# Kernel tuning notes

Hardware: AMD Instinct MI355X
Metric: run time of the kernel (lower is better)

## Reference

```python
import jax, jax.numpy as jnp
import numpy as np

B, H, W, D = 4, 64, 64, 256
NH = 8
HD = D // NH        # 32
R = 2               # reduction_ratio
SCALE = 1.0 / np.sqrt(HD).astype(np.float32)
EPS = 1e-5


def _layernorm(x, g, b):
    m = jnp.mean(x, axis=-1, keepdims=True)
    v = jnp.mean((x - m) ** 2, axis=-1, keepdims=True)
    return (x - m) * jax.lax.rsqrt(v + EPS) * g + b


def setup_inputs() -> dict:
    key = jax.random.key(0)
    ks = jax.random.split(key, 8)
    s = 0.02
    return {
        "x": jax.random.normal(ks[0], (B, H, W, D), jnp.float32),
        "de": jax.random.normal(ks[1], (B, H, W, D), jnp.float32),  # unused by module
        "ln1_g": jnp.ones((D,), jnp.float32),
        "ln1_b": jnp.zeros((D,), jnp.float32),
        "Wq": jax.random.normal(ks[2], (D, D), jnp.float32) * s,
        "bq": jnp.zeros((D,), jnp.float32),
        "Wk": jax.random.normal(ks[3], (D, D), jnp.float32) * s,
        "bk": jnp.zeros((D,), jnp.float32),
        "Wv": jax.random.normal(ks[4], (D, D), jnp.float32) * s,
        "bv": jnp.zeros((D,), jnp.float32),
        "Wmean": jax.random.normal(ks[5], (D, D), jnp.float32) * s,  # no bias
        "ln2_g": jnp.ones((D,), jnp.float32),
        "ln2_b": jnp.zeros((D,), jnp.float32),
        "Wo": jax.random.normal(ks[6], (D, D), jnp.float32) * s,
        "bo": jnp.zeros((D,), jnp.float32),
    }


def reference(x, de, ln1_g, ln1_b, Wq, bq, Wk, bk, Wv, bv, Wmean, ln2_g, ln2_b, Wo, bo):
    b, h, w, d = x.shape
    identity = x
    x_norm = _layernorm(x, ln1_g, ln1_b)
    q = x_norm @ Wq + bq                                   # [b,h,w,d]
    # shift_size == 0 -> no roll. Block-mean pool K/V by factor R.
    x_red = jnp.mean(x.reshape(b, h // R, R, w // R, R, d), axis=(2, 4))  # [b,h/R,w/R,d]
    x_red = x_red @ Wmean
    x_red_norm = _layernorm(x_red, ln2_g, ln2_b)
    k = x_red_norm @ Wk + bk
    v = x_red_norm @ Wv + bv
    # split heads: [b, NH, N, HD]
    qf = q.reshape(b, h * w, NH, HD).transpose(0, 2, 1, 3)
    kf = k.reshape(b, (h // R) * (w // R), NH, HD).transpose(0, 2, 1, 3)
    vf = v.reshape(b, (h // R) * (w // R), NH, HD).transpose(0, 2, 1, 3)
    attn = jax.nn.softmax(jnp.einsum('bhqd,bhkd->bhqk', qf, kf) * SCALE, axis=-1)
    out = jnp.einsum('bhqk,bhkd->bhqd', attn, vf)          # [b,NH,N,HD]
    out = out.transpose(0, 2, 1, 3).reshape(b, h, w, d)
    out = out @ Wo + bo
    out = out + identity
    return out, attn
```

## Files before the change

### kernel.cpp

```cpp
#include <hip/hip_runtime.h>

typedef __bf16 bf16x8 __attribute__((ext_vector_type(8)));
typedef __bf16 bf16x4 __attribute__((ext_vector_type(4)));
typedef float f32x4 __attribute__((ext_vector_type(4)));

#define SCALE 0.17677669529663687f

__global__ __launch_bounds__(256) void castw_kernel(
    const float* __restrict__ W0, const float* __restrict__ W1,
    const float* __restrict__ W2, const float* __restrict__ W3,
    const float* __restrict__ W4,
    __bf16* __restrict__ T0, __bf16* __restrict__ T1,
    __bf16* __restrict__ T2, __bf16* __restrict__ T3,
    __bf16* __restrict__ T4) {
  int which = blockIdx.x >> 8;
  const float* W = which == 0 ? W0 : which == 1 ? W1 : which == 2 ? W2 : which == 3 ? W3 : W4;
  __bf16* T = which == 0 ? T0 : which == 1 ? T1 : which == 2 ? T2 : which == 3 ? T3 : T4;
  int id = (blockIdx.x & 255) * 256 + threadIdx.x;
  int kk = id >> 8, n = id & 255;
  T[n * 256 + kk] = (__bf16)W[id];
}

__global__ __launch_bounds__(256) void ln_fp32_kernel(const float* __restrict__ in,
    const float* __restrict__ g, const float* __restrict__ bb,
    __bf16* __restrict__ out) {
  int wid = (blockIdx.x * 256 + threadIdx.x) >> 6;
  int lane = threadIdx.x & 63;
  const float4 v = *(const float4*)(in + (size_t)wid * 256 + lane * 4);
  float s = v.x + v.y + v.z + v.w;
  #pragma unroll
  for (int off = 32; off; off >>= 1) s += __shfl_down(s, off);
  float mean = __shfl(s, 0) * (1.0f / 256.0f);
  float dx = v.x - mean, dy = v.y - mean, dz = v.z - mean, dw = v.w - mean;
  float vs = dx * dx + dy * dy + dz * dz + dw * dw;
  #pragma unroll
  for (int off = 32; off; off >>= 1) vs += __shfl_down(vs, off);
  float rstd = rsqrtf(__shfl(vs, 0) * (1.0f / 256.0f) + 1e-5f);
  const float4 gg = *(const float4*)(g + lane * 4);
  const float4 bv = *(const float4*)(bb + lane * 4);
  bf16x4 o4;
  o4[0] = (__bf16)(dx * rstd * gg.x + bv.x);
  o4[1] = (__bf16)(dy * rstd * gg.y + bv.y);
  o4[2] = (__bf16)(dz * rstd * gg.z + bv.z);
  o4[3] = (__bf16)(dw * rstd * gg.w + bv.w);
  *(bf16x4*)(out + (size_t)wid * 256 + lane * 4) = o4;
}

__global__ __launch_bounds__(256) void ln_bf16_kernel(const __bf16* __restrict__ in,
    const float* __restrict__ g, const float* __restrict__ bb,
    __bf16* __restrict__ out) {
  int wid = (blockIdx.x * 256 + threadIdx.x) >> 6;
  int lane = threadIdx.x & 63;
  bf16x4 iv = *(const bf16x4*)(in + (size_t)wid * 256 + lane * 4);
  float vx = (float)iv[0], vy = (float)iv[1], vz = (float)iv[2], vw = (float)iv[3];
  float s = vx + vy + vz + vw;
  #pragma unroll
  for (int off = 32; off; off >>= 1) s += __shfl_down(s, off);
  float mean = __shfl(s, 0) * (1.0f / 256.0f);
  float dx = vx - mean, dy = vy - mean, dz = vz - mean, dw = vw - mean;
  float vs = dx * dx + dy * dy + dz * dz + dw * dw;
  #pragma unroll
  for (int off = 32; off; off >>= 1) vs += __shfl_down(vs, off);
  float rstd = rsqrtf(__shfl(vs, 0) * (1.0f / 256.0f) + 1e-5f);
  const float4 gg = *(const float4*)(g + lane * 4);
  const float4 bv = *(const float4*)(bb + lane * 4);
  bf16x4 o4;
  o4[0] = (__bf16)(dx * rstd * gg.x + bv.x);
  o4[1] = (__bf16)(dy * rstd * gg.y + bv.y);
  o4[2] = (__bf16)(dz * rstd * gg.z + bv.z);
  o4[3] = (__bf16)(dw * rstd * gg.w + bv.w);
  *(bf16x4*)(out + (size_t)wid * 256 + lane * 4) = o4;
}

__global__ __launch_bounds__(256) void pool_kernel(const float* __restrict__ x,
    __bf16* __restrict__ xp) {
  int idx = blockIdx.x * 256 + threadIdx.x;
  int t = idx >> 6, c4 = (idx & 63) << 2;
  int b = t >> 10, rem = t & 1023;
  int i = rem >> 5, j = rem & 31;
  size_t base = ((size_t)b * 4096 + i * 128 + j * 2) * 256 + c4;
  float4 a0 = *(const float4*)(x + base);
  float4 a1 = *(const float4*)(x + base + 256);
  float4 a2 = *(const float4*)(x + base + 16384);
  float4 a3 = *(const float4*)(x + base + 16640);
  bf16x4 o4;
  o4[0] = (__bf16)(0.25f * (a0.x + a1.x + a2.x + a3.x));
  o4[1] = (__bf16)(0.25f * (a0.y + a1.y + a2.y + a3.y));
  o4[2] = (__bf16)(0.25f * (a0.z + a1.z + a2.z + a3.z));
  o4[3] = (__bf16)(0.25f * (a0.w + a1.w + a2.w + a3.w));
  *(bf16x4*)(xp + (size_t)t * 256 + c4) = o4;
}

__global__ __launch_bounds__(256) void gemm_mfma(
    const __bf16* __restrict__ A, const __bf16* __restrict__ Wt,
    const float* __restrict__ bias, const float* __restrict__ resid,
    void* __restrict__ Cout, int mode) {
  const int tid = threadIdx.x;
  const int w = tid >> 6, l = tid & 63;
  const int col = l & 15, quad = l >> 4;
  const int row0 = blockIdx.x * 64 + w * 16;
  const int col0 = blockIdx.y * 64;
  f32x4 acc[4] = {{0.f,0.f,0.f,0.f},{0.f,0.f,0.f,0.f},{0.f,0.f,0.f,0.f},{0.f,0.f,0.f,0.f}};
  const __bf16* ap = A + (size_t)(row0 + col) * 256 + quad * 8;
  #pragma unroll
  for (int ks = 0; ks < 8; ++ks) {
    bf16x8 af = *(const bf16x8*)(ap + ks * 32);
    #pragma unroll
    for (int n = 0; n < 4; ++n) {
      bf16x8 bf = *(const bf16x8*)(Wt + (size_t)(col0 + n * 16 + col) * 256 + ks * 32 + quad * 8);
      acc[n] = __builtin_amdgcn_mfma_f32_16x16x32_bf16(af, bf, acc[n], 0, 0, 0);
    }
  }
  const int rbase = row0 + quad * 4;
  #pragma unroll
  for (int n = 0; n < 4; ++n) {
    const int cc = col0 + n * 16 + col;
    const float bv = bias ? bias[cc] : 0.0f;
    if (mode == 0) {
      __bf16* C = (__bf16*)Cout;
      #pragma unroll
      for (int r = 0; r < 4; ++r)
        C[(size_t)(rbase + r) * 256 + cc] = (__bf16)(acc[n][r] + bv);
    } else if (mode == 1) {
      __bf16* C = (__bf16*)Cout;
      const int bb2 = rbase >> 10, tl = rbase & 1023;
      bf16x4 o4;
      #pragma unroll
      for (int r = 0; r < 4; ++r) o4[r] = (__bf16)(acc[n][r] + bv);
      *(bf16x4*)(C + ((size_t)(bb2 * 256 + cc)) * 1024 + tl) = o4;
    } else {
      float* C = (float*)Cout;
      #pragma unroll
      for (int r = 0; r < 4; ++r) {
        size_t off = (size_t)(rbase + r) * 256 + cc;
        C[off] = acc[n][r] + bv + resid[off];
      }
    }
  }
}

__device__ __forceinline__ int swz(int row, int c) {
  return row * 1024 + (c ^ ((row & 7) << 2));
}

__global__ __launch_bounds__(256) void attn_fused(
    const __bf16* __restrict__ q, const __bf16* __restrict__ kb,
    const __bf16* __restrict__ vT, float* __restrict__ attn,
    __bf16* __restrict__ oat) {
  __shared__ float Ss[16 * 1024];
  __shared__ float part[64 * 32];
  __shared__ float inv_s[16];
  const int tid = threadIdx.x;
  const int w = tid >> 6, l = tid & 63;
  const int col = l & 15, quad = l >> 4;
  const int bh = blockIdx.y, b = bh >> 3, h = bh & 7;
  const int q0 = blockIdx.x * 16;

  bf16x8 qf = *(const bf16x8*)(q + ((size_t)(b * 4096 + q0 + col)) * 256 + h * 32 + quad * 8);
  const __bf16* kbase = kb + ((size_t)(b * 1024 + col)) * 256 + h * 32 + quad * 8;
  #pragma unroll 4
  for (int t = 0; t < 16; ++t) {
    int j0 = w * 256 + t * 16;
    bf16x8 kf = *(const bf16x8*)(kbase + (size_t)j0 * 256);
    f32x4 c = {0.f, 0.f, 0.f, 0.f};
    c = __builtin_amdgcn_mfma_f32_16x16x32_bf16(qf, kf, c, 0, 0, 0);
    #pragma unroll
    for (int r = 0; r < 4; ++r)
      Ss[swz(quad * 4 + r, j0 + col)] = c[r] * SCALE;
  }
  __syncthreads();

  #pragma unroll
  for (int rr = 0; rr < 4; ++rr) {
    int row = w * 4 + rr;
    float4 v4[4];
    float m = -1e30f;
    #pragma unroll
    for (int i = 0; i < 4; ++i) {
      v4[i] = *(const float4*)(&Ss[swz(row, i * 256 + l * 4)]);
      m = fmaxf(m, fmaxf(fmaxf(v4[i].x, v4[i].y), fmaxf(v4[i].z, v4[i].w)));
    }
    #pragma unroll
    for (int off = 32; off; off >>= 1) m = fmaxf(m, __shfl_down(m, off));
    m = __shfl(m, 0);
    float s = 0.f;
    #pragma unroll
    for (int i = 0; i < 4; ++i) {
      v4[i].x = __expf(v4[i].x - m); v4[i].y = __expf(v4[i].y - m);
      v4[i].z = __expf(v4[i].z - m); v4[i].w = __expf(v4[i].w - m);
      s += v4[i].x + v4[i].y + v4[i].z + v4[i].w;
    }
    #pragma unroll
    for (int off = 32; off; off >>= 1) s += __shfl_down(s, off);
    if (l == 0) inv_s[row] = 1.0f / __shfl(s, 0);
    #pragma unroll
    for (int i = 0; i < 4; ++i)
      *(float4*)(&Ss[swz(row, i * 256 + l * 4)]) = v4[i];
  }
  __syncthreads();

  f32x4 a0 = {0.f, 0.f, 0.f, 0.f}, a1 = {0.f, 0.f, 0.f, 0.f};
  const __bf16* v0p = vT + ((size_t)(b * 256 + h * 32 + col)) * 1024;
  const __bf16* v1p = v0p + 16 * 1024;
  #pragma unroll 2
  for (int s8 = 0; s8 < 8; ++s8) {
    int k0 = w * 256 + s8 * 32;
    int c0 = k0 + quad * 8;
    f32x4 p0 = *(const f32x4*)(&Ss[swz(col, c0)]);
    f32x4 p1 = *(const f32x4*)(&Ss[swz(col, c0 + 4)]);
    bf16x8 af;
    af[0] = (__bf16)p0[0]; af[1] = (__bf16)p0[1]; af[2] = (__bf16)p0[2]; af[3] = (__bf16)p0[3];
    af[4] = (__bf16)p1[0]; af[5] = (__bf16)p1[1]; af[6] = (__bf16)p1[2]; af[7] = (__bf16)p1[3];
    bf16x8 b0 = *(const bf16x8*)(v0p + k0 + quad * 8);
    bf16x8 b1 = *(const bf16x8*)(v1p + k0 + quad * 8);
    a0 = __builtin_amdgcn_mfma_f32_16x16x32_bf16(af, b0, a0, 0, 0, 0);
    a1 = __builtin_amdgcn_mfma_f32_16x16x32_bf16(af, b1, a1, 0, 0, 0);
  }

  #pragma unroll
  for (int r = 0; r < 4; ++r) {
    part[(w * 16 + quad * 4 + r) * 32 + col] = a0[r];
    part[(w * 16 + quad * 4 + r) * 32 + 16 + col] = a1[r];
  }
  __syncthreads();
  int idx = tid;
  #pragma unroll
  for (int it = 0; it < 2; ++it, idx += 256) {
    int row = idx >> 5, d = idx & 31;
    float sum = (part[row * 32 + d] + part[(16 + row) * 32 + d]
               + part[(32 + row) * 32 + d] + part[(48 + row) * 32 + d]) * inv_s[row];
    oat[((size_t)(b * 4096 + q0 + row)) * 256 + h * 32 + d] = (__bf16)sum;
  }

  float* abase = attn + ((size_t)bh * 4096 + q0) * 1024;
  int c4 = tid * 4;
  #pragma unroll 4
  for (int row = 0; row < 16; ++row) {
    f32x4 pv = *(const f32x4*)(&Ss[swz(row, c4)]);
    float iv = inv_s[row];
    pv[0] *= iv; pv[1] *= iv; pv[2] *= iv; pv[3] *= iv;
    __builtin_nontemporal_store(pv, (f32x4*)(abase + (size_t)row * 1024 + c4));
  }
}

extern "C" void kernel_launch(void* const* d_in, const int* in_sizes, int n_in,
                              void* d_out, int out_size, void* d_ws, size_t ws_size,
                              hipStream_t stream) {
  (void)in_sizes; (void)n_in; (void)out_size; (void)ws_size;
  const float* x     = (const float*)d_in[0];
  const float* ln1_g = (const float*)d_in[2];
  const float* ln1_b = (const float*)d_in[3];
  const float* Wq    = (const float*)d_in[4];
  const float* bq    = (const float*)d_in[5];
  const float* Wk    = (const float*)d_in[6];
  const float* bk    = (const float*)d_in[7];
  const float* Wv    = (const float*)d_in[8];
  const float* bv    = (const float*)d_in[9];
  const float* Wmean = (const float*)d_in[10];
  const float* ln2_g = (const float*)d_in[11];
  const float* ln2_b = (const float*)d_in[12];
  const float* Wo    = (const float*)d_in[13];
  const float* bo    = (const float*)d_in[14];

  float* out  = (float*)d_out;
  float* attn = out + 4194304;

  __bf16* w0   = (__bf16*)d_ws;
  __bf16* xn   = w0;
  __bf16* qb   = w0 + 4194304;
  __bf16* oat  = w0 + 8388608;
  __bf16* xp   = w0 + 12582912;
  __bf16* xrm  = w0 + 13631488;
  __bf16* xr   = w0 + 14680064;
  __bf16* kbuf = w0 + 15728640;
  __bf16* vTb  = w0 + 16777216;
  __bf16* WtQ  = w0 + 17825792;
  __bf16* WtK  = WtQ + 65536;
  __bf16* WtV  = WtK + 65536;
  __bf16* WtM  = WtV + 65536;
  __bf16* WtO  = WtM + 65536;

  castw_kernel<<<1280, 256, 0, stream>>>(Wq, Wk, Wv, Wmean, Wo, WtQ, WtK, WtV, WtM, WtO);

  ln_fp32_kernel<<<4096, 256, 0, stream>>>(x, ln1_g, ln1_b, xn);
  gemm_mfma<<<dim3(256, 4), 256, 0, stream>>>(xn, WtQ, bq, nullptr, qb, 0);
  pool_kernel<<<1024, 256, 0, stream>>>(x, xp);
  gemm_mfma<<<dim3(64, 4), 256, 0, stream>>>(xp, WtM, nullptr, nullptr, xrm, 0);
  ln_bf16_kernel<<<1024, 256, 0, stream>>>(xrm, ln2_g, ln2_b, xr);
  gemm_mfma<<<dim3(64, 4), 256, 0, stream>>>(xr, WtK, bk, nullptr, kbuf, 0);
  gemm_mfma<<<dim3(64, 4), 256, 0, stream>>>(xr, WtV, bv, nullptr, vTb, 1);
  attn_fused<<<dim3(256, 32), 256, 0, stream>>>(qb, kbuf, vTb, attn, oat);
  gemm_mfma<<<dim3(256, 4), 256, 0, stream>>>(oat, WtO, bo, x, (void*)out, 2);
}
```

Before: 741.0 us.

## Merge prep kernels, fuse Wmean GEMM with LayerNorm, and batch K/V GEMMs

Reduces ten launches to five. The weight cast, LN1 and pooling now run as one block-partitioned kernel. The Q projection shares a launch with a Wmean GEMM that computes full 256-wide rows per warp and applies LN2 in registers, which removes the xrm round trip and the separate LN kernel. K and V GEMMs share one launch. The attention kernel now writes the attn matrix before the PV MFMA loop, which may overlap the big store with compute, and the GEMM mode becomes a template parameter. The fused Wmean path uses 16 accumulators per lane, which raises register pressure, and its per-element bf16 stores are uncoalesced.

Result: no change. 744.9 us (+0.5%).

```diff
diff --git a/kernel.cpp b/kernel.cpp
--- a/kernel.cpp
+++ b/kernel.cpp
@@ -6,100 +6,15 @@
 
 #define SCALE 0.17677669529663687f
 
-__global__ __launch_bounds__(256) void castw_kernel(
-    const float* __restrict__ W0, const float* __restrict__ W1,
-    const float* __restrict__ W2, const float* __restrict__ W3,
-    const float* __restrict__ W4,
-    __bf16* __restrict__ T0, __bf16* __restrict__ T1,
-    __bf16* __restrict__ T2, __bf16* __restrict__ T3,
-    __bf16* __restrict__ T4) {
-  int which = blockIdx.x >> 8;
-  const float* W = which == 0 ? W0 : which == 1 ? W1 : which == 2 ? W2 : which == 3 ? W3 : W4;
-  __bf16* T = which == 0 ? T0 : which == 1 ? T1 : which == 2 ? T2 : which == 3 ? T3 : T4;
-  int id = (blockIdx.x & 255) * 256 + threadIdx.x;
-  int kk = id >> 8, n = id & 255;
-  T[n * 256 + kk] = (__bf16)W[id];
-}
-
-__global__ __launch_bounds__(256) void ln_fp32_kernel(const float* __restrict__ in,
-    const float* __restrict__ g, const float* __restrict__ bb,
-    __bf16* __restrict__ out) {
-  int wid = (blockIdx.x * 256 + threadIdx.x) >> 6;
-  int lane = threadIdx.x & 63;
-  const float4 v = *(const float4*)(in + (size_t)wid * 256 + lane * 4);
-  float s = v.x + v.y + v.z + v.w;
-  #pragma unroll
-  for (int off = 32; off; off >>= 1) s += __shfl_down(s, off);
-  float mean = __shfl(s, 0) * (1.0f / 256.0f);
-  float dx = v.x - mean, dy = v.y - mean, dz = v.z - mean, dw = v.w - mean;
-  float vs = dx * dx + dy * dy + dz * dz + dw * dw;
-  #pragma unroll
-  for (int off = 32; off; off >>= 1) vs += __shfl_down(vs, off);
-  float rstd = rsqrtf(__shfl(vs, 0) * (1.0f / 256.0f) + 1e-5f);
-  const float4 gg = *(const float4*)(g + lane * 4);
-  const float4 bv = *(const float4*)(bb + lane * 4);
-  bf16x4 o4;
-  o4[0] = (__bf16)(dx * rstd * gg.x + bv.x);
-  o4[1] = (__bf16)(dy * rstd * gg.y + bv.y);
-  o4[2] = (__bf16)(dz * rstd * gg.z + bv.z);
-  o4[3] = (__bf16)(dw * rstd * gg.w + bv.w);
-  *(bf16x4*)(out + (size_t)wid * 256 + lane * 4) = o4;
-}
-
-__global__ __launch_bounds__(256) void ln_bf16_kernel(const __bf16* __restrict__ in,
-    const float* __restrict__ g, const float* __restrict__ bb,
-    __bf16* __restrict__ out) {
-  int wid = (blockIdx.x * 256 + threadIdx.x) >> 6;
-  int lane = threadIdx.x & 63;
-  bf16x4 iv = *(const bf16x4*)(in + (size_t)wid * 256 + lane * 4);
-  float vx = (float)iv[0], vy = (float)iv[1], vz = (float)iv[2], vw = (float)iv[3];
-  float s = vx + vy + vz + vw;
-  #pragma unroll
-  for (int off = 32; off; off >>= 1) s += __shfl_down(s, off);
-  float mean = __shfl(s, 0) * (1.0f / 256.0f);
-  float dx = vx - mean, dy = vy - mean, dz = vz - mean, dw = vw - mean;
-  float vs = dx * dx + dy * dy + dz * dz + dw * dw;
-  #pragma unroll
-  for (int off = 32; off; off >>= 1) vs += __shfl_down(vs, off);
-  float rstd = rsqrtf(__shfl(vs, 0) * (1.0f / 256.0f) + 1e-5f);
-  const float4 gg = *(const float4*)(g + lane * 4);
-  const float4 bv = *(const float4*)(bb + lane * 4);
-  bf16x4 o4;
-  o4[0] = (__bf16)(dx * rstd * gg.x + bv.x);
-  o4[1] = (__bf16)(dy * rstd * gg.y + bv.y);
-  o4[2] = (__bf16)(dz * rstd * gg.z + bv.z);
-  o4[3] = (__bf16)(dw * rstd * gg.w + bv.w);
-  *(bf16x4*)(out + (size_t)wid * 256 + lane * 4) = o4;
-}
-
-__global__ __launch_bounds__(256) void pool_kernel(const float* __restrict__ x,
-    __bf16* __restrict__ xp) {
-  int idx = blockIdx.x * 256 + threadIdx.x;
-  int t = idx >> 6, c4 = (idx & 63) << 2;
-  int b = t >> 10, rem = t & 1023;
-  int i = rem >> 5, j = rem & 31;
-  size_t base = ((size_t)b * 4096 + i * 128 + j * 2) * 256 + c4;
-  float4 a0 = *(const float4*)(x + base);
-  float4 a1 = *(const float4*)(x + base + 256);
-  float4 a2 = *(const float4*)(x + base + 16384);
-  float4 a3 = *(const float4*)(x + base + 16640);
-  bf16x4 o4;
-  o4[0] = (__bf16)(0.25f * (a0.x + a1.x + a2.x + a3.x));
-  o4[1] = (__bf16)(0.25f * (a0.y + a1.y + a2.y + a3.y));
-  o4[2] = (__bf16)(0.25f * (a0.z + a1.z + a2.z + a3.z));
-  o4[3] = (__bf16)(0.25f * (a0.w + a1.w + a2.w + a3.w));
-  *(bf16x4*)(xp + (size_t)t * 256 + c4) = o4;
-}
-
-__global__ __launch_bounds__(256) void gemm_mfma(
-    const __bf16* __restrict__ A, const __bf16* __restrict__ Wt,
-    const float* __restrict__ bias, const float* __restrict__ resid,
-    void* __restrict__ Cout, int mode) {
-  const int tid = threadIdx.x;
+template<int MODE>
+__device__ __forceinline__ void gemm_body(const __bf16* __restrict__ A,
+    const __bf16* __restrict__ Wt, const float* __restrict__ bias,
+    const float* __restrict__ resid, void* __restrict__ Cout,
+    int bx, int by, int tid) {
   const int w = tid >> 6, l = tid & 63;
   const int col = l & 15, quad = l >> 4;
-  const int row0 = blockIdx.x * 64 + w * 16;
-  const int col0 = blockIdx.y * 64;
+  const int row0 = bx * 64 + w * 16;
+  const int col0 = by * 64;
   f32x4 acc[4] = {{0.f,0.f,0.f,0.f},{0.f,0.f,0.f,0.f},{0.f,0.f,0.f,0.f},{0.f,0.f,0.f,0.f}};
   const __bf16* ap = A + (size_t)(row0 + col) * 256 + quad * 8;
   #pragma unroll
@@ -116,12 +31,12 @@
   for (int n = 0; n < 4; ++n) {
     const int cc = col0 + n * 16 + col;
     const float bv = bias ? bias[cc] : 0.0f;
-    if (mode == 0) {
+    if (MODE == 0) {
       __bf16* C = (__bf16*)Cout;
       #pragma unroll
       for (int r = 0; r < 4; ++r)
         C[(size_t)(rbase + r) * 256 + cc] = (__bf16)(acc[n][r] + bv);
-    } else if (mode == 1) {
+    } else if (MODE == 1) {
       __bf16* C = (__bf16*)Cout;
       const int bb2 = rbase >> 10, tl = rbase & 1023;
       bf16x4 o4;
@@ -139,6 +54,131 @@
   }
 }
 
+__global__ __launch_bounds__(256) void prep_kernel(
+    const float* __restrict__ W0, const float* __restrict__ W1,
+    const float* __restrict__ W2, const float* __restrict__ W3,
+    const float* __restrict__ W4,
+    __bf16* __restrict__ T0, __bf16* __restrict__ T1,
+    __bf16* __restrict__ T2, __bf16* __restrict__ T3,
+    __bf16* __restrict__ T4,
+    const float* __restrict__ x, const float* __restrict__ g1,
+    const float* __restrict__ b1, __bf16* __restrict__ xn,
+    __bf16* __restrict__ xp) {
+  const int blk = blockIdx.x, tid = threadIdx.x;
+  if (blk < 1280) {
+    int which = blk >> 8;
+    const float* W = which == 0 ? W0 : which == 1 ? W1 : which == 2 ? W2 : which == 3 ? W3 : W4;
+    __bf16* T = which == 0 ? T0 : which == 1 ? T1 : which == 2 ? T2 : which == 3 ? T3 : T4;
+    int id = (blk & 255) * 256 + tid;
+    int kk = id >> 8, n = id & 255;
+    T[n * 256 + kk] = (__bf16)W[id];
+  } else if (blk < 5376) {
+    int wid = ((blk - 1280) * 256 + tid) >> 6;
+    int lane = tid & 63;
+    const float4 v = *(const float4*)(x + (size_t)wid * 256 + lane * 4);
+    float s = v.x + v.y + v.z + v.w;
+    #pragma unroll
+    for (int off = 32; off; off >>= 1) s += __shfl_down(s, off);
+    float mean = __shfl(s, 0) * (1.0f / 256.0f);
+    float dx = v.x - mean, dy = v.y - mean, dz = v.z - mean, dw = v.w - mean;
+    float vs = dx * dx + dy * dy + dz * dz + dw * dw;
+    #pragma unroll
+    for (int off = 32; off; off >>= 1) vs += __shfl_down(vs, off);
+    float rstd = rsqrtf(__shfl(vs, 0) * (1.0f / 256.0f) + 1e-5f);
+    const float4 gg = *(const float4*)(g1 + lane * 4);
+    const float4 bv = *(const float4*)(b1 + lane * 4);
+    bf16x4 o4;
+    o4[0] = (__bf16)(dx * rstd * gg.x + bv.x);
+    o4[1] = (__bf16)(dy * rstd * gg.y + bv.y);
+    o4[2] = (__bf16)(dz * rstd * gg.z + bv.z);
+    o4[3] = (__bf16)(dw * rstd * gg.w + bv.w);
+    *(bf16x4*)(xn + (size_t)wid * 256 + lane * 4) = o4;
+  } else {
+    int idx = (blk - 5376) * 256 + tid;
+    int t = idx >> 6, c4 = (idx & 63) << 2;
+    int b = t >> 10, rem = t & 1023;
+    int i = rem >> 5, j = rem & 31;
+    size_t base = ((size_t)b * 4096 + i * 128 + j * 2) * 256 + c4;
+    float4 a0 = *(const float4*)(x + base);
+    float4 a1 = *(const float4*)(x + base + 256);
+    float4 a2 = *(const float4*)(x + base + 16384);
+    float4 a3 = *(const float4*)(x + base + 16640);
+    bf16x4 o4;
+    o4[0] = (__bf16)(0.25f * (a0.x + a1.x + a2.x + a3.x));
+    o4[1] = (__bf16)(0.25f * (a0.y + a1.y + a2.y + a3.y));
+    o4[2] = (__bf16)(0.25f * (a0.z + a1.z + a2.z + a3.z));
+    o4[3] = (__bf16)(0.25f * (a0.w + a1.w + a2.w + a3.w));
+    *(bf16x4*)(xp + (size_t)t * 256 + c4) = o4;
+  }
+}
+
+__global__ __launch_bounds__(256) void qm_kernel(
+    const __bf16* __restrict__ xn, const __bf16* __restrict__ WtQ,
+    const float* __restrict__ bq, __bf16* __restrict__ qb,
+    const __bf16* __restrict__ xp, const __bf16* __restrict__ WtM,
+    const float* __restrict__ g2, const float* __restrict__ b2,
+    __bf16* __restrict__ xr) {
+  const int blk = blockIdx.x, tid = threadIdx.x;
+  if (blk < 1024) {
+    gemm_body<0>(xn, WtQ, bq, nullptr, qb, blk & 255, blk >> 8, tid);
+    return;
+  }
+  const int w = tid >> 6, l = tid & 63;
+  const int col = l & 15, quad = l >> 4;
+  const int row0 = (blk - 1024) * 64 + w * 16;
+  f32x4 acc[16];
+  #pragma unroll
+  for (int n = 0; n < 16; ++n) acc[n] = (f32x4){0.f, 0.f, 0.f, 0.f};
+  const __bf16* ap = xp + (size_t)(row0 + col) * 256 + quad * 8;
+  #pragma unroll
+  for (int ks = 0; ks < 8; ++ks) {
+    bf16x8 af = *(const bf16x8*)(ap + ks * 32);
+    #pragma unroll
+    for (int n = 0; n < 16; ++n) {
+      bf16x8 bf = *(const bf16x8*)(WtM + (size_t)(n * 16 + col) * 256 + ks * 32 + quad * 8);
+      acc[n] = __builtin_amdgcn_mfma_f32_16x16x32_bf16(af, bf, acc[n], 0, 0, 0);
+    }
+  }
+  #pragma unroll
+  for (int r = 0; r < 4; ++r) {
+    float s = 0.f;
+    #pragma unroll
+    for (int n = 0; n < 16; ++n) s += acc[n][r];
+    #pragma unroll
+    for (int m = 1; m < 16; m <<= 1) s += __shfl_xor(s, m);
+    float mean = s * (1.0f / 256.0f);
+    float vs = 0.f;
+    #pragma unroll
+    for (int n = 0; n < 16; ++n) { float d = acc[n][r] - mean; vs += d * d; }
+    #pragma unroll
+    for (int m = 1; m < 16; m <<= 1) vs += __shfl_xor(vs, m);
+    float rstd = rsqrtf(vs * (1.0f / 256.0f) + 1e-5f);
+    int row = row0 + quad * 4 + r;
+    #pragma unroll
+    for (int n = 0; n < 16; ++n) {
+      int cc = n * 16 + col;
+      xr[(size_t)row * 256 + cc] = (__bf16)((acc[n][r] - mean) * rstd * g2[cc] + b2[cc]);
+    }
+  }
+}
+
+__global__ __launch_bounds__(256) void kv_kernel(
+    const __bf16* __restrict__ xr, const __bf16* __restrict__ WtK,
+    const float* __restrict__ bk, __bf16* __restrict__ kbuf,
+    const __bf16* __restrict__ WtV, const float* __restrict__ bv,
+    __bf16* __restrict__ vTb) {
+  const int blk = blockIdx.x, tid = threadIdx.x;
+  if (blk < 256) gemm_body<0>(xr, WtK, bk, nullptr, kbuf, blk & 63, blk >> 6, tid);
+  else { int k = blk - 256; gemm_body<1>(xr, WtV, bv, nullptr, vTb, k & 63, k >> 6, tid); }
+}
+
+__global__ __launch_bounds__(256) void o_kernel(
+    const __bf16* __restrict__ oat, const __bf16* __restrict__ WtO,
+    const float* __restrict__ bo, const float* __restrict__ resid,
+    float* __restrict__ out) {
+  gemm_body<2>(oat, WtO, bo, resid, out, blockIdx.x, blockIdx.y, threadIdx.x);
+}
+
 __device__ __forceinline__ int swz(int row, int c) {
   return row * 1024 + (c ^ ((row & 7) << 2));
 }
@@ -198,6 +238,18 @@
       *(float4*)(&Ss[swz(row, i * 256 + l * 4)]) = v4[i];
   }
   __syncthreads();
+
+  {
+    float* abase = attn + ((size_t)bh * 4096 + q0) * 1024;
+    int c4 = tid * 4;
+    #pragma unroll 4
+    for (int row = 0; row < 16; ++row) {
+      f32x4 pv = *(const f32x4*)(&Ss[swz(row, c4)]);
+      float iv = inv_s[row];
+      pv[0] *= iv; pv[1] *= iv; pv[2] *= iv; pv[3] *= iv;
+      __builtin_nontemporal_store(pv, (f32x4*)(abase + (size_t)row * 1024 + c4));
+    }
+  }
 
   f32x4 a0 = {0.f, 0.f, 0.f, 0.f}, a1 = {0.f, 0.f, 0.f, 0.f};
   const __bf16* v0p = vT + ((size_t)(b * 256 + h * 32 + col)) * 1024;
@@ -230,16 +282,6 @@
     float sum = (part[row * 32 + d] + part[(16 + row) * 32 + d]
                + part[(32 + row) * 32 + d] + part[(48 + row) * 32 + d]) * inv_s[row];
     oat[((size_t)(b * 4096 + q0 + row)) * 256 + h * 32 + d] = (__bf16)sum;
-  }
-
-  float* abase = attn + ((size_t)bh * 4096 + q0) * 1024;
-  int c4 = tid * 4;
-  #pragma unroll 4
-  for (int row = 0; row < 16; ++row) {
-    f32x4 pv = *(const f32x4*)(&Ss[swz(row, c4)]);
-    float iv = inv_s[row];
-    pv[0] *= iv; pv[1] *= iv; pv[2] *= iv; pv[3] *= iv;
-    __builtin_nontemporal_store(pv, (f32x4*)(abase + (size_t)row * 1024 + c4));
   }
 }
 
@@ -270,7 +312,6 @@
   __bf16* qb   = w0 + 4194304;
   __bf16* oat  = w0 + 8388608;
   __bf16* xp   = w0 + 12582912;
-  __bf16* xrm  = w0 + 13631488;
   __bf16* xr   = w0 + 14680064;
   __bf16* kbuf = w0 + 15728640;
   __bf16* vTb  = w0 + 16777216;
@@ -280,15 +321,11 @@
   __bf16* WtM  = WtV + 65536;
   __bf16* WtO  = WtM + 65536;
 
-  castw_kernel<<<1280, 256, 0, stream>>>(Wq, Wk, Wv, Wmean, Wo, WtQ, WtK, WtV, WtM, WtO);
-
-  ln_fp32_kernel<<<4096, 256, 0, stream>>>(x, ln1_g, ln1_b, xn);
-  gemm_mfma<<<dim3(256, 4), 256, 0, stream>>>(xn, WtQ, bq, nullptr, qb, 0);
-  pool_kernel<<<1024, 256, 0, stream>>>(x, xp);
-  gemm_mfma<<<dim3(64, 4), 256, 0, stream>>>(xp, WtM, nullptr, nullptr, xrm, 0);
-  ln_bf16_kernel<<<1024, 256, 0, stream>>>(xrm, ln2_g, ln2_b, xr);
-  gemm_mfma<<<dim3(64, 4), 256, 0, stream>>>(xr, WtK, bk, nullptr, kbuf, 0);
-  gemm_mfma<<<dim3(64, 4), 256, 0, stream>>>(xr, WtV, bv, nullptr, vTb, 1);
+  prep_kernel<<<6400, 256, 0, stream>>>(Wq, Wk, Wv, Wmean, Wo,
+                                        WtQ, WtK, WtV, WtM, WtO,
+                                        x, ln1_g, ln1_b, xn, xp);
+  qm_kernel<<<1088, 256, 0, stream>>>(xn, WtQ, bq, qb, xp, WtM, ln2_g, ln2_b, xr);
+  kv_kernel<<<512, 256, 0, stream>>>(xr, WtK, bk, kbuf, WtV, bv, vTb);
   attn_fused<<<dim3(256, 32), 256, 0, stream>>>(qb, kbuf, vTb, attn, oat);
-  gemm_mfma<<<dim3(256, 4), 256, 0, stream>>>(oat, WtO, bo, x, (void*)out, 2);
-}
+  o_kernel<<<dim3(256, 4), 256, 0, stream>>>(oat, WtO, bo, x, out);
+}
```
